# Kernel tuning notes

Measured on AMD Instinct MI355X. Metric: run time of the kernel, lower is better.

Reference implementation:

```python
import jax, jax.numpy as jnp
import numpy as np

ALPHA = 0.2  # LeakyReLU negative slope
NEG_INF = -9e15


def setup_inputs() -> dict:
    key = jax.random.key(0)
    k1, k2, k3, k4 = jax.random.split(key, 4)
    N, IN_F, OUT_F, H = 8192, 256, 128, 2
    HD = OUT_F // H
    h = jax.random.normal(k1, (N, IN_F), dtype=jnp.float32)
    adj = jax.random.randint(k2, (N, N), 0, 2, dtype=jnp.int32)
    # xavier_uniform with gain=1.414
    g = 1.414
    limW = g * np.sqrt(6.0 / (IN_F + HD))
    W = jax.random.uniform(k3, (H, IN_F, HD), jnp.float32, -limW, limW)
    lima = g * np.sqrt(6.0 / (2 * HD + 1))
    a = jax.random.uniform(k4, (H, 2 * HD, 1), jnp.float32, -lima, lima)
    return {"h": h, "adj": adj, "W": W, "a": a}


def reference(h, adj, W, a):
    # Wh: (H, N, HD)
    Wh = jnp.einsum('ni,hid->hnd', h, W)
    HD = W.shape[-1]
    a1 = a[:, :HD, 0]   # (H, HD) -> applied to Wh_i
    a2 = a[:, HD:, 0]   # (H, HD) -> applied to Wh_j
    # a . [Wh_i || Wh_j] == a1.Wh_i + a2.Wh_j ; avoids the (N,N,2HD) tensor
    f1 = jnp.einsum('hnd,hd->hn', Wh, a1)  # (H, N)
    f2 = jnp.einsum('hnd,hd->hn', Wh, a2)  # (H, N)
    e = jax.nn.leaky_relu(f1[:, :, None] + f2[:, None, :], ALPHA)  # (H, N, N)
    mask = (adj > 0)[None, :, :]
    e = jnp.where(mask, e, NEG_INF)
    attention = jax.nn.softmax(e, axis=-1)  # (H, N, N)
    # dropout is identity in eval mode
    h_prime = jnp.einsum('hnm,hmd->hnd', attention, Wh)  # (H, N, HD)
    N = h.shape[0]
    h_prime = jnp.transpose(h_prime, (1, 0, 2)).reshape(N, -1)  # concat heads
    return jax.nn.elu(h_prime)
```

## Files before the change

kernel.cpp:

```cpp
#include <hip/hip_runtime.h>
#include <hip/hip_bf16.h>
#include <stdint.h>

#define N_NODES 8192
#define IN_F    256
#define HD      64
#define NH      2
#define MS      8
#define NT      ((N_NODES / MS) / 64)
#define ALPHA   0.2f

typedef __attribute__((ext_vector_type(8))) short bf16x8s;
typedef __attribute__((ext_vector_type(4))) float f32x4;

#define OFF_U      0
#define OFF_WFRAG  4096
#define OFF_F1     69632
#define OFF_F2     135168
#define OFF_F2MAX  200704
#define OFF_G2     200960
#define OFF_WHB    332032
#define OFF_OP     2429184
#define OFF_LP     35983616
#define OFF_MB     36507648

__device__ __forceinline__ unsigned short f2bf(float x) {
  union { float f; uint32_t u; } c; c.f = x;
  uint32_t r = c.u + 0x7FFFu + ((c.u >> 16) & 1u);
  return (unsigned short)(r >> 16);
}
__device__ __forceinline__ short f2bfs(float x) {
  __hip_bfloat16 b = __float2bfloat16(x);
  return __builtin_bit_cast(short, b);
}

__global__ __launch_bounds__(256) void gat_pack_kernel(const int* __restrict__ adj,
    unsigned long long* __restrict__ mbits)
{
  int w = threadIdx.x >> 6, l = threadIdx.x & 63;
  int r = blockIdx.x * 4 + w;
  const int4* src = (const int4*)(adj + (size_t)r * N_NODES) + l;
  unsigned long long* dst = mbits + (size_t)r * 128;
#pragma unroll 2
  for (int c = 0; c < 32; ++c) {
    int4 v = src[c * 64];
    unsigned long long b0 = __ballot(v.x > 0);
    unsigned long long b1 = __ballot(v.y > 0);
    unsigned long long b2 = __ballot(v.z > 0);
    unsigned long long b3 = __ballot(v.w > 0);
    if (l == 0) {
      *(ulonglong2*)(dst + c * 4)     = make_ulonglong2(b0, b1);
      *(ulonglong2*)(dst + c * 4 + 2) = make_ulonglong2(b2, b3);
    }
  }
}

__global__ void gat_prep_kernel(const float* __restrict__ W, const float* __restrict__ a,
                                float* __restrict__ u, unsigned short* __restrict__ wfrag)
{
  int idx = blockIdx.x * 256 + threadIdx.x;
  if (idx < 32768) {
    int j = idx & 7, lane = (idx >> 3) & 63, ks = (idx >> 9) & 7, Dt = idx >> 12;
    int k  = ks * 32 + ((lane >> 4) << 3) + j;
    int dp = Dt * 16 + (lane & 15);
    int hh = dp >> 6, d = dp & 63;
    wfrag[idx] = f2bf(W[(size_t)(hh * IN_F + k) * HD + d]);
  } else if (idx < 32768 + NH * 2 * IN_F) {
    int i2 = idx - 32768;
    int i = i2 & 255, v = (i2 >> 8) & 1, h = i2 >> 9;
    const float* Wp = W + (size_t)(h * IN_F + i) * HD;
    const float* ap = a + h * 2 * HD + v * HD;
    float s = 0.f;
    for (int d = 0; d < HD; ++d) s += Wp[d] * ap[d];
    u[(h * 2 + v) * IN_F + i] = s;
  }
}

__global__ __launch_bounds__(256) void gat_f12_kernel(const float* __restrict__ hmat,
    const float* __restrict__ u, float* __restrict__ f1, float* __restrict__ f2,
    float2* __restrict__ g2)
{
  int n = blockIdx.x * 4 + (threadIdx.x >> 6);
  int l = threadIdx.x & 63;
  float4 hv = *(const float4*)(hmat + (size_t)n * IN_F + l * 4);
  float s[4];
#pragma unroll
  for (int q = 0; q < 4; ++q) {
    float4 uv = *(const float4*)(u + q * IN_F + l * 4);
    s[q] = hv.x * uv.x + hv.y * uv.y + hv.z * uv.z + hv.w * uv.w;
  }
#pragma unroll
  for (int off = 1; off < 64; off <<= 1) {
#pragma unroll
    for (int q = 0; q < 4; ++q) s[q] += __shfl_xor(s[q], off);
  }
  if (l == 0) {
    f1[n] = s[0];           f2[n] = s[1];
    f1[N_NODES + n] = s[2]; f2[N_NODES + n] = s[3];
    g2[n]           = make_float2(__expf(s[1]), __expf(ALPHA * s[1]));
    g2[N_NODES + n] = make_float2(__expf(s[3]), __expf(ALPHA * s[3]));
  }
}

__global__ void gat_f2max_kernel(const float* __restrict__ f2, float* __restrict__ f2m)
{
  int h = blockIdx.x;
  float m = -1e30f;
  for (int i = threadIdx.x; i < N_NODES; i += 256) m = fmaxf(m, f2[h * N_NODES + i]);
#pragma unroll
  for (int off = 1; off < 64; off <<= 1) m = fmaxf(m, __shfl_xor(m, off));
  __shared__ float red[4];
  if ((threadIdx.x & 63) == 0) red[threadIdx.x >> 6] = m;
  __syncthreads();
  if (threadIdx.x == 0) f2m[h] = fmaxf(fmaxf(red[0], red[1]), fmaxf(red[2], red[3]));
}

__global__ __launch_bounds__(256) void gat_wh_kernel(const float* __restrict__ hmat,
    const unsigned short* __restrict__ wfrag, unsigned short* __restrict__ whb)
{
  int tid = threadIdx.x;
  int w = tid >> 6, l = tid & 63;
  int n0 = blockIdx.x * 64;
  int row = n0 + w * 16 + (l & 15);
  f32x4 acc[8] = {};
#pragma unroll
  for (int ks = 0; ks < 8; ++ks) {
    const float* ap = hmat + (size_t)row * IN_F + ks * 32 + ((l >> 4) << 3);
    float av[8];
    *(float4*)&av[0] = *(const float4*)ap;
    *(float4*)&av[4] = *(const float4*)(ap + 4);
    bf16x8s af;
#pragma unroll
    for (int j = 0; j < 8; ++j) af[j] = f2bfs(av[j]);
#pragma unroll
    for (int Dt = 0; Dt < 8; ++Dt) {
      bf16x8s bfv = *(const bf16x8s*)(wfrag + ((size_t)(Dt * 8 + ks) * 64 + l) * 8);
      acc[Dt] = __builtin_amdgcn_mfma_f32_16x16x32_bf16(af, bfv, acc[Dt], 0, 0, 0);
    }
  }
  int Tm = blockIdx.x;
  int s  = w >> 1;
  int lb = ((w & 1) * 2 + ((l >> 4) >> 1)) * 16 + (l & 15);
  int jh = (l >> 4) & 1;
#pragma unroll
  for (int Dt = 0; Dt < 8; ++Dt) {
    int hh = Dt >> 2, D = Dt & 3;
    ushort4 pk;
    pk.x = f2bf(acc[Dt][0]); pk.y = f2bf(acc[Dt][1]);
    pk.z = f2bf(acc[Dt][2]); pk.w = f2bf(acc[Dt][3]);
    size_t off = ((((size_t)(hh * 128 + Tm) * 2 + s) * 4 + D) * 64 + lb) * 8 + jh * 4;
    *(ushort4*)(whb + off) = pk;
  }
}

__global__ __launch_bounds__(256, 2) void gat_attn_kernel(
    const unsigned long long* __restrict__ mbits, const unsigned short* __restrict__ whb,
    const float* __restrict__ f1, const float2* __restrict__ g2,
    const float* __restrict__ f2max, float* __restrict__ Opart, float* __restrict__ Lpart)
{
  int bx = blockIdx.x;
  int split = bx & (MS - 1);
  int T = bx >> 3;
  int tid = threadIdx.x;
  int w = tid >> 6, l = tid & 63;
  int n0 = T * 128;
  int rbase = n0 + w * 16 + (l & 15);
  int mbase = split * (N_NODES / MS);
  int koff = (l >> 4) << 3;

  float E1[NH][2], Ea[NH][2];
#pragma unroll
  for (int h = 0; h < NH; ++h)
#pragma unroll
    for (int rg = 0; rg < 2; ++rg) {
      float f1v = f1[h * N_NODES + rbase + rg * 64];
      float tm  = f1v + f2max[h];
      float mrow = fmaxf(tm, ALPHA * tm);
      E1[h][rg] = __expf(f1v - mrow);
      Ea[h][rg] = __expf(ALPHA * f1v - mrow);
    }

  __shared__ float4 gl[2][512];
  __shared__ uint4  wbuf[1024];

  {
    const float4* s0 = (const float4*)(g2 + mbase);
    const float4* s1 = (const float4*)(g2 + N_NODES + mbase);
    gl[0][tid] = s0[tid]; gl[0][tid + 256] = s0[tid + 256];
    gl[1][tid] = s1[tid]; gl[1][tid + 256] = s1[tid + 256];
  }

  int cb0 = mbase >> 8;
  const ulonglong2* mp0 = (const ulonglong2*)mbits + (size_t)rbase * 64 + cb0 * 2;
  const ulonglong2* mp1 = mp0 + (size_t)64 * 64;

  const uint4* ws0 = (const uint4*)(whb + ((size_t)(mbase >> 6)) * 4096);
  const uint4* ws1 = (const uint4*)(whb + ((size_t)(128 + (mbase >> 6))) * 4096);

  ulonglong2 cmA0 = mp0[0], cmA1 = mp0[1], cmB0 = mp1[0], cmB1 = mp1[1];
  ulonglong2 nmA0 = mp0[2], nmA1 = mp0[3], nmB0 = mp1[2], nmB1 = mp1[3];
  uint4 rw0 = ws0[tid], rw1 = ws0[tid + 256];
  uint4 rw2 = ws1[tid], rw3 = ws1[tid + 256];

  f32x4 acc[NH][2][4] = {};
  float lsum[NH][2] = {};

  for (int mt = 0; mt < NT; ++mt) {
    __syncthreads();
    wbuf[tid]       = rw0; wbuf[tid + 256] = rw1;
    wbuf[tid + 512] = rw2; wbuf[tid + 768] = rw3;
    if (mt + 1 < NT) {
      const uint4* wp0 = ws0 + (size_t)(mt + 1) * 512;
      const uint4* wp1 = ws1 + (size_t)(mt + 1) * 512;
      rw0 = wp0[tid]; rw1 = wp0[tid + 256];
      rw2 = wp1[tid]; rw3 = wp1[tid + 256];
    }
    if (mt && (mt & 3) == 0) {
      cmA0 = nmA0; cmA1 = nmA1; cmB0 = nmB0; cmB1 = nmB1;
      int cb = (mt >> 2) + 1;
      if (cb < NT / 4) {
        nmA0 = mp0[cb * 2]; nmA1 = mp0[cb * 2 + 1];
        nmB0 = mp1[cb * 2]; nmB1 = mp1[cb * 2 + 1];
      }
    }
    __syncthreads();

    int shbase = ((mt & 3) << 4) + ((l >> 4) << 1);
    bf16x8s afA[NH][2], afB[NH][2];
#pragma unroll
    for (int s = 0; s < 2; ++s) {
      int sh = shbase + s * 8;
      uint32_t t0 = (uint32_t)(cmA0.x >> sh), t1 = (uint32_t)(cmA0.y >> sh);
      uint32_t t2 = (uint32_t)(cmA1.x >> sh), t3 = (uint32_t)(cmA1.y >> sh);
      uint32_t u0 = (uint32_t)(cmB0.x >> sh), u1 = (uint32_t)(cmB0.y >> sh);
      uint32_t u2 = (uint32_t)(cmB1.x >> sh), u3 = (uint32_t)(cmB1.y >> sh);
#pragma unroll
      for (int h = 0; h < NH; ++h) {
        const float4* gp = &gl[h][(mt * 64 + s * 32 + koff) >> 1];
        float psA = 0.f, psB = 0.f;
#pragma unroll
        for (int k = 0; k < 4; ++k) {
          float4 gv = gp[k];
          uint32_t txA = (k & 1) ? t2 : t0, tyA = (k & 1) ? t3 : t1;
          uint32_t txB = (k & 1) ? u2 : u0, tyB = (k & 1) ? u3 : u1;
          int kb = k >> 1;
          float vA0 = fmaxf(E1[h][0] * gv.x, Ea[h][0] * gv.y);
          float vA1 = fmaxf(E1[h][0] * gv.z, Ea[h][0] * gv.w);
          float vB0 = fmaxf(E1[h][1] * gv.x, Ea[h][1] * gv.y);
          float vB1 = fmaxf(E1[h][1] * gv.z, Ea[h][1] * gv.w);
          float pA0 = ((txA >> kb) & 1) ? vA0 : 0.f;
          float pA1 = ((tyA >> kb) & 1) ? vA1 : 0.f;
          float pB0 = ((txB >> kb) & 1) ? vB0 : 0.f;
          float pB1 = ((tyB >> kb) & 1) ? vB1 : 0.f;
          psA += pA0 + pA1;  psB += pB0 + pB1;
          afA[h][s][2 * k] = f2bfs(pA0); afA[h][s][2 * k + 1] = f2bfs(pA1);
          afB[h][s][2 * k] = f2bfs(pB0); afB[h][s][2 * k + 1] = f2bfs(pB1);
        }
        lsum[h][0] += psA; lsum[h][1] += psB;
      }
    }

#pragma unroll
    for (int h = 0; h < NH; ++h) {
      const unsigned short* lb = (const unsigned short*)wbuf + h * 4096;
#pragma unroll
      for (int s = 0; s < 2; ++s)
#pragma unroll
        for (int D = 0; D < 4; ++D) {
          bf16x8s bfv = *(const bf16x8s*)&lb[(s * 4 + D) * 512 + l * 8];
          acc[h][0][D] = __builtin_amdgcn_mfma_f32_16x16x32_bf16(afA[h][s], bfv, acc[h][0][D], 0, 0, 0);
          acc[h][1][D] = __builtin_amdgcn_mfma_f32_16x16x32_bf16(afB[h][s], bfv, acc[h][1][D], 0, 0, 0);
        }
    }
  }

#pragma unroll
  for (int h = 0; h < NH; ++h)
#pragma unroll
    for (int rg = 0; rg < 2; ++rg) {
      float ls = lsum[h][rg];
      ls += __shfl_xor(ls, 16);
      ls += __shfl_xor(ls, 32);
      if (l < 16) Lpart[((size_t)(split * NH + h) << 13) + n0 + rg * 64 + w * 16 + l] = ls;
      float* op = Opart + (size_t)(split * NH + h) * N_NODES * HD;
#pragma unroll
      for (int D = 0; D < 4; ++D)
#pragma unroll
        for (int r = 0; r < 4; ++r) {
          int orow = n0 + rg * 64 + w * 16 + ((l >> 4) << 2) + r;
          op[(size_t)orow * HD + D * 16 + (l & 15)] = acc[h][rg][D][r];
        }
    }
}

__global__ __launch_bounds__(256) void gat_final_kernel(const float* __restrict__ Opart,
    const float* __restrict__ Lpart, float* __restrict__ out)
{
  int idx = blockIdx.x * 256 + threadIdx.x;
  int n = idx >> 7, c = idx & 127;
  int h = c >> 6, d = c & 63;
  float v = 0.f, ls = 0.f;
#pragma unroll
  for (int sp = 0; sp < MS; ++sp) {
    v  += Opart[((size_t)(sp * NH + h) * N_NODES + n) * HD + d];
    ls += Lpart[(size_t)(sp * NH + h) * N_NODES + n];
  }
  float r = v / fmaxf(ls, 1e-30f);
  out[idx] = (r > 0.f) ? r : (__expf(r) - 1.f);
}

extern "C" void kernel_launch(void* const* d_in, const int* in_sizes, int n_in,
                              void* d_out, int out_size, void* d_ws, size_t ws_size,
                              hipStream_t stream)
{
  const float* hmat = (const float*)d_in[0];
  const int*   adj  = (const int*)d_in[1];
  const float* W    = (const float*)d_in[2];
  const float* a    = (const float*)d_in[3];
  float* out = (float*)d_out;
  char* ws = (char*)d_ws;

  float* u             = (float*)(ws + OFF_U);
  unsigned short* wfrg = (unsigned short*)(ws + OFF_WFRAG);
  float* f1            = (float*)(ws + OFF_F1);
  float* f2            = (float*)(ws + OFF_F2);
  float* f2m           = (float*)(ws + OFF_F2MAX);
  float2* g2           = (float2*)(ws + OFF_G2);
  unsigned short* whb  = (unsigned short*)(ws + OFF_WHB);
  float* Opart         = (float*)(ws + OFF_OP);
  float* Lpart         = (float*)(ws + OFF_LP);
  unsigned long long* mbits = (unsigned long long*)(ws + OFF_MB);

  gat_pack_kernel <<<N_NODES / 4, 256, 0, stream>>>(adj, mbits);
  gat_prep_kernel <<<132, 256, 0, stream>>>(W, a, u, wfrg);
  gat_f12_kernel  <<<N_NODES / 4, 256, 0, stream>>>(hmat, u, f1, f2, g2);
  gat_f2max_kernel<<<NH, 256, 0, stream>>>(f2, f2m);
  gat_wh_kernel   <<<N_NODES / 64, 256, 0, stream>>>(hmat, wfrg, whb);
  gat_attn_kernel <<<64 * MS, 256, 0, stream>>>(mbits, whb, f1, g2, f2m, Opart, Lpart);
  gat_final_kernel<<<out_size / 256, 256, 0, stream>>>(Opart, Lpart, out);
}
```

Before: 132.6 us.

## Fuse adjacency bit-packing into attention kernel with in-loop prefetch of second chunk

Drops the separate pack kernel, which read the int32 adjacency matrix and wrote a packed bitmask to global memory. Each attention block now reads its own 128x1024 adjacency tile and ballots it into a shared-memory bitmask. The first 512 columns are packed up front. The second half is loaded inside the main loop and packed after each iteration's MFMA work, so those loads overlap compute. This removes one launch and the bitmask write and re-read, but adds register pressure and shared memory to the attention kernel.

```diff
diff --git a/kernel.cpp b/kernel.cpp
--- a/kernel.cpp
+++ b/kernel.cpp
@@ -7,7 +7,9 @@
 #define HD      64
 #define NH      2
 #define MS      8
-#define NT      ((N_NODES / MS) / 64)
+#define SLICE   1024
+#define CHUNK   512
+#define NT      16
 #define ALPHA   0.2f
 
 typedef __attribute__((ext_vector_type(8))) short bf16x8s;
@@ -22,7 +24,6 @@
 #define OFF_WHB    332032
 #define OFF_OP     2429184
 #define OFF_LP     35983616
-#define OFF_MB     36507648
 
 __device__ __forceinline__ unsigned short f2bf(float x) {
   union { float f; uint32_t u; } c; c.f = x;
@@ -32,27 +33,6 @@
 __device__ __forceinline__ short f2bfs(float x) {
   __hip_bfloat16 b = __float2bfloat16(x);
   return __builtin_bit_cast(short, b);
-}
-
-__global__ __launch_bounds__(256) void gat_pack_kernel(const int* __restrict__ adj,
-    unsigned long long* __restrict__ mbits)
-{
-  int w = threadIdx.x >> 6, l = threadIdx.x & 63;
-  int r = blockIdx.x * 4 + w;
-  const int4* src = (const int4*)(adj + (size_t)r * N_NODES) + l;
-  unsigned long long* dst = mbits + (size_t)r * 128;
-#pragma unroll 2
-  for (int c = 0; c < 32; ++c) {
-    int4 v = src[c * 64];
-    unsigned long long b0 = __ballot(v.x > 0);
-    unsigned long long b1 = __ballot(v.y > 0);
-    unsigned long long b2 = __ballot(v.z > 0);
-    unsigned long long b3 = __ballot(v.w > 0);
-    if (l == 0) {
-      *(ulonglong2*)(dst + c * 4)     = make_ulonglong2(b0, b1);
-      *(ulonglong2*)(dst + c * 4 + 2) = make_ulonglong2(b2, b3);
-    }
-  }
 }
 
 __global__ void gat_prep_kernel(const float* __restrict__ W, const float* __restrict__ a,
@@ -153,8 +133,33 @@
   }
 }
 
+#define LOADB(dst, b, cb) { \
+  const int* _p = abase + (size_t)(w * 32 + (b) * 4) * N_NODES + (cb) + 4 * l; \
+  dst##0 = *(const int4*)_p;                  dst##1 = *(const int4*)(_p + 256); \
+  dst##2 = *(const int4*)(_p + N_NODES);      dst##3 = *(const int4*)(_p + N_NODES + 256); \
+  dst##4 = *(const int4*)(_p + 2 * N_NODES);  dst##5 = *(const int4*)(_p + 2 * N_NODES + 256); \
+  dst##6 = *(const int4*)(_p + 3 * N_NODES);  dst##7 = *(const int4*)(_p + 3 * N_NODES + 256); \
+}
+#define PACKR(v0, v1, rowexpr, buf) { \
+  unsigned long long _b0 = __ballot(v0.x > 0), _b1 = __ballot(v0.y > 0); \
+  unsigned long long _b2 = __ballot(v0.z > 0), _b3 = __ballot(v0.w > 0); \
+  unsigned long long _b4 = __ballot(v1.x > 0), _b5 = __ballot(v1.y > 0); \
+  unsigned long long _b6 = __ballot(v1.z > 0), _b7 = __ballot(v1.w > 0); \
+  if (l == 0) { \
+    ulonglong2* _mp = (ulonglong2*)&maskbuf[buf][rowexpr][0]; \
+    _mp[0] = make_ulonglong2(_b0, _b1); _mp[1] = make_ulonglong2(_b2, _b3); \
+    _mp[2] = make_ulonglong2(_b4, _b5); _mp[3] = make_ulonglong2(_b6, _b7); \
+  } \
+}
+#define PACKB(src, b, buf) { \
+  PACKR(src##0, src##1, w * 32 + (b) * 4 + 0, buf); \
+  PACKR(src##2, src##3, w * 32 + (b) * 4 + 1, buf); \
+  PACKR(src##4, src##5, w * 32 + (b) * 4 + 2, buf); \
+  PACKR(src##6, src##7, w * 32 + (b) * 4 + 3, buf); \
+}
+
 __global__ __launch_bounds__(256, 2) void gat_attn_kernel(
-    const unsigned long long* __restrict__ mbits, const unsigned short* __restrict__ whb,
+    const int* __restrict__ adj, const unsigned short* __restrict__ whb,
     const float* __restrict__ f1, const float2* __restrict__ g2,
     const float* __restrict__ f2max, float* __restrict__ Opart, float* __restrict__ Lpart)
 {
@@ -165,8 +170,34 @@
   int w = tid >> 6, l = tid & 63;
   int n0 = T * 128;
   int rbase = n0 + w * 16 + (l & 15);
-  int mbase = split * (N_NODES / MS);
+  int mbase = split * SLICE;
   int koff = (l >> 4) << 3;
+
+  __shared__ float4 gl[2][512];
+  __shared__ uint4  wbuf[1024];
+  __shared__ unsigned long long maskbuf[2][128][8];
+
+  {
+    const float4* s0 = (const float4*)(g2 + mbase);
+    const float4* s1 = (const float4*)(g2 + N_NODES + mbase);
+    gl[0][tid] = s0[tid]; gl[0][tid + 256] = s0[tid + 256];
+    gl[1][tid] = s1[tid]; gl[1][tid + 256] = s1[tid + 256];
+  }
+
+  const int* abase = adj + (size_t)n0 * N_NODES + mbase;
+
+  {
+    int4 sA0, sA1, sA2, sA3, sA4, sA5, sA6, sA7;
+    int4 sB0, sB1, sB2, sB3, sB4, sB5, sB6, sB7;
+    LOADB(sA, 0, 0); LOADB(sB, 1, 0);
+    PACKB(sA, 0, 0); LOADB(sA, 2, 0);
+    PACKB(sB, 1, 0); LOADB(sB, 3, 0);
+    PACKB(sA, 2, 0); LOADB(sA, 4, 0);
+    PACKB(sB, 3, 0); LOADB(sB, 5, 0);
+    PACKB(sA, 4, 0); LOADB(sA, 6, 0);
+    PACKB(sB, 5, 0); LOADB(sB, 7, 0);
+    PACKB(sA, 6, 0); PACKB(sB, 7, 0);
+  }
 
   float E1[NH][2], Ea[NH][2];
 #pragma unroll
@@ -180,62 +211,50 @@
       Ea[h][rg] = __expf(ALPHA * f1v - mrow);
     }
 
-  __shared__ float4 gl[2][512];
-  __shared__ uint4  wbuf[1024];
-
-  {
-    const float4* s0 = (const float4*)(g2 + mbase);
-    const float4* s1 = (const float4*)(g2 + N_NODES + mbase);
-    gl[0][tid] = s0[tid]; gl[0][tid + 256] = s0[tid + 256];
-    gl[1][tid] = s1[tid]; gl[1][tid + 256] = s1[tid + 256];
-  }
-
-  int cb0 = mbase >> 8;
-  const ulonglong2* mp0 = (const ulonglong2*)mbits + (size_t)rbase * 64 + cb0 * 2;
-  const ulonglong2* mp1 = mp0 + (size_t)64 * 64;
-
   const uint4* ws0 = (const uint4*)(whb + ((size_t)(mbase >> 6)) * 4096);
   const uint4* ws1 = (const uint4*)(whb + ((size_t)(128 + (mbase >> 6))) * 4096);
-
-  ulonglong2 cmA0 = mp0[0], cmA1 = mp0[1], cmB0 = mp1[0], cmB1 = mp1[1];
-  ulonglong2 nmA0 = mp0[2], nmA1 = mp0[3], nmB0 = mp1[2], nmB1 = mp1[3];
   uint4 rw0 = ws0[tid], rw1 = ws0[tid + 256];
   uint4 rw2 = ws1[tid], rw3 = ws1[tid + 256];
 
   f32x4 acc[NH][2][4] = {};
   float lsum[NH][2] = {};
+  ulonglong2 cmA0, cmA1, cmB0, cmB1;
 
   for (int mt = 0; mt < NT; ++mt) {
+    int ch = mt >> 3, tc = mt & 7, q = tc & 3, g = tc >> 2;
+
     __syncthreads();
     wbuf[tid]       = rw0; wbuf[tid + 256] = rw1;
     wbuf[tid + 512] = rw2; wbuf[tid + 768] = rw3;
+    __syncthreads();
+
+    int4 sA0, sA1, sA2, sA3, sA4, sA5, sA6, sA7;
+    if (mt < 8) LOADB(sA, tc, CHUNK);
+
+    if (q == 0) {
+      const ulonglong2* m0 = (const ulonglong2*)&maskbuf[ch][w * 16 + (l & 15)][g * 4];
+      cmA0 = m0[0]; cmA1 = m0[1];
+      const ulonglong2* m1 = (const ulonglong2*)&maskbuf[ch][w * 16 + 64 + (l & 15)][g * 4];
+      cmB0 = m1[0]; cmB1 = m1[1];
+    }
+
     if (mt + 1 < NT) {
       const uint4* wp0 = ws0 + (size_t)(mt + 1) * 512;
       const uint4* wp1 = ws1 + (size_t)(mt + 1) * 512;
       rw0 = wp0[tid]; rw1 = wp0[tid + 256];
       rw2 = wp1[tid]; rw3 = wp1[tid + 256];
     }
-    if (mt && (mt & 3) == 0) {
-      cmA0 = nmA0; cmA1 = nmA1; cmB0 = nmB0; cmB1 = nmB1;
-      int cb = (mt >> 2) + 1;
-      if (cb < NT / 4) {
-        nmA0 = mp0[cb * 2]; nmA1 = mp0[cb * 2 + 1];
-        nmB0 = mp1[cb * 2]; nmB1 = mp1[cb * 2 + 1];
-      }
-    }
-    __syncthreads();
-
-    int shbase = ((mt & 3) << 4) + ((l >> 4) << 1);
-    bf16x8s afA[NH][2], afB[NH][2];
-#pragma unroll
-    for (int s = 0; s < 2; ++s) {
-      int sh = shbase + s * 8;
-      uint32_t t0 = (uint32_t)(cmA0.x >> sh), t1 = (uint32_t)(cmA0.y >> sh);
-      uint32_t t2 = (uint32_t)(cmA1.x >> sh), t3 = (uint32_t)(cmA1.y >> sh);
-      uint32_t u0 = (uint32_t)(cmB0.x >> sh), u1 = (uint32_t)(cmB0.y >> sh);
-      uint32_t u2 = (uint32_t)(cmB1.x >> sh), u3 = (uint32_t)(cmB1.y >> sh);
-#pragma unroll
-      for (int h = 0; h < NH; ++h) {
+
+#pragma unroll
+    for (int h = 0; h < NH; ++h) {
+      bf16x8s afA[2], afB[2];
+#pragma unroll
+      for (int s = 0; s < 2; ++s) {
+        int sh = (q << 4) + ((l >> 4) << 1) + (s << 3);
+        uint32_t t0 = (uint32_t)(cmA0.x >> sh), t1 = (uint32_t)(cmA0.y >> sh);
+        uint32_t t2 = (uint32_t)(cmA1.x >> sh), t3 = (uint32_t)(cmA1.y >> sh);
+        uint32_t u0 = (uint32_t)(cmB0.x >> sh), u1 = (uint32_t)(cmB0.y >> sh);
+        uint32_t u2 = (uint32_t)(cmB1.x >> sh), u3 = (uint32_t)(cmB1.y >> sh);
         const float4* gp = &gl[h][(mt * 64 + s * 32 + koff) >> 1];
         float psA = 0.f, psB = 0.f;
 #pragma unroll
@@ -253,25 +272,23 @@
           float pB0 = ((txB >> kb) & 1) ? vB0 : 0.f;
           float pB1 = ((tyB >> kb) & 1) ? vB1 : 0.f;
           psA += pA0 + pA1;  psB += pB0 + pB1;
-          afA[h][s][2 * k] = f2bfs(pA0); afA[h][s][2 * k + 1] = f2bfs(pA1);
-          afB[h][s][2 * k] = f2bfs(pB0); afB[h][s][2 * k + 1] = f2bfs(pB1);
+          afA[s][2 * k] = f2bfs(pA0); afA[s][2 * k + 1] = f2bfs(pA1);
+          afB[s][2 * k] = f2bfs(pB0); afB[s][2 * k + 1] = f2bfs(pB1);
         }
         lsum[h][0] += psA; lsum[h][1] += psB;
       }
-    }
-
-#pragma unroll
-    for (int h = 0; h < NH; ++h) {
       const unsigned short* lb = (const unsigned short*)wbuf + h * 4096;
 #pragma unroll
       for (int s = 0; s < 2; ++s)
 #pragma unroll
         for (int D = 0; D < 4; ++D) {
           bf16x8s bfv = *(const bf16x8s*)&lb[(s * 4 + D) * 512 + l * 8];
-          acc[h][0][D] = __builtin_amdgcn_mfma_f32_16x16x32_bf16(afA[h][s], bfv, acc[h][0][D], 0, 0, 0);
-          acc[h][1][D] = __builtin_amdgcn_mfma_f32_16x16x32_bf16(afB[h][s], bfv, acc[h][1][D], 0, 0, 0);
+          acc[h][0][D] = __builtin_amdgcn_mfma_f32_16x16x32_bf16(afA[s], bfv, acc[h][0][D], 0, 0, 0);
+          acc[h][1][D] = __builtin_amdgcn_mfma_f32_16x16x32_bf16(afB[s], bfv, acc[h][1][D], 0, 0, 0);
         }
     }
+
+    if (mt < 8) PACKB(sA, tc, 1);
   }
 
 #pragma unroll
@@ -329,13 +346,11 @@
   unsigned short* whb  = (unsigned short*)(ws + OFF_WHB);
   float* Opart         = (float*)(ws + OFF_OP);
   float* Lpart         = (float*)(ws + OFF_LP);
-  unsigned long long* mbits = (unsigned long long*)(ws + OFF_MB);
-
-  gat_pack_kernel <<<N_NODES / 4, 256, 0, stream>>>(adj, mbits);
+
   gat_prep_kernel <<<132, 256, 0, stream>>>(W, a, u, wfrg);
   gat_f12_kernel  <<<N_NODES / 4, 256, 0, stream>>>(hmat, u, f1, f2, g2);
   gat_f2max_kernel<<<NH, 256, 0, stream>>>(f2, f2m);
   gat_wh_kernel   <<<N_NODES / 64, 256, 0, stream>>>(hmat, wfrg, whb);
-  gat_attn_kernel <<<64 * MS, 256, 0, stream>>>(mbits, whb, f1, g2, f2m, Opart, Lpart);
+  gat_attn_kernel <<<64 * MS, 256, 0, stream>>>(adj, whb, f1, g2, f2m, Opart, Lpart);
   gat_final_kernel<<<out_size / 256, 256, 0, stream>>>(Opart, Lpart, out);
 }
```

Measured after the change: 111.5 us. 1.19x faster.
